# Kernel tuning notes

Hardware: AMD Instinct MI355X
Metric: run time of the kernel (lower is better)

Reference implementation:

```python
import jax, jax.numpy as jnp
import numpy as np

E = 1024      # emb_dim
H = 16        # num_heads
DH = E // H   # per-head atten_dim
B = 2
T = 2048


def _layernorm(x, scale, shift, eps=1e-5):
    mean = x.mean(axis=-1, keepdims=True)
    var = ((x - mean) ** 2).mean(axis=-1, keepdims=True)  # unbiased=False
    return scale * (x - mean) / jnp.sqrt(var + eps) + shift


def _gelu(x):
    # Faithful to source: tanh(sqrt(2/pi)*x + 0.044715*x^3)  (no sqrt on cubic term)
    c = jnp.sqrt(jnp.asarray(2.0 / jnp.pi, x.dtype))
    return 0.5 * x * (1.0 + jnp.tanh(c * x + 0.044715 * x ** 3))


def setup_inputs() -> dict:
    key = jax.random.key(0)
    ks = jax.random.split(key, 12)
    s = 0.02
    return {
        "x":     jax.random.normal(ks[0], (B, T, E), jnp.float32),
        "Wq":    jax.random.normal(ks[1], (H, E, DH), jnp.float32) * s,
        "Wk":    jax.random.normal(ks[2], (H, E, DH), jnp.float32) * s,
        "Wv":    jax.random.normal(ks[3], (H, E, DH), jnp.float32) * s,
        "fc_w":  jax.random.normal(ks[4], (E, E), jnp.float32) * s,
        "fc_b":  jnp.zeros((E,), jnp.float32),
        "ln1_s": jnp.ones((E,), jnp.float32),
        "ln1_b": jnp.zeros((E,), jnp.float32),
        "ln2_s": jnp.ones((E,), jnp.float32),
        "ln2_b": jnp.zeros((E,), jnp.float32),
        "ff_w1": jax.random.normal(ks[5], (E, 4 * E), jnp.float32) * s,
        "ff_b1": jnp.zeros((4 * E,), jnp.float32),
        "ff_w2": jax.random.normal(ks[6], (4 * E, E), jnp.float32) * s,
        "ff_b2": jnp.zeros((E,), jnp.float32),
    }


def _attention(x, Wq, Wk, Wv, fc_w, fc_b):
    b, t, _ = x.shape
    q = jnp.einsum("bte,hed->bhtd", x, Wq)
    k = jnp.einsum("bte,hed->bhtd", x, Wk)
    v = jnp.einsum("bte,hed->bhtd", x, Wv)
    scores = jnp.einsum("bhtd,bhsd->bhts", q, k)
    causal = jnp.triu(jnp.ones((t, t), bool), 1)
    scores = jnp.where(causal, -jnp.inf, scores)
    w = jax.nn.softmax(scores / jnp.sqrt(jnp.asarray(DH, x.dtype)), axis=-1)
    ctx = jnp.einsum("bhts,bhsd->bhtd", w, v)
    # faithful quirk from source: per-head transpose(1,2) then reshape(b, T, d_out)
    ctx = jnp.swapaxes(ctx, 2, 3).reshape(b, H, t, DH)
    concat = ctx.transpose(0, 2, 1, 3).reshape(b, t, E)
    return concat @ fc_w + fc_b


def reference(x, Wq, Wk, Wv, fc_w, fc_b, ln1_s, ln1_b, ln2_s, ln2_b,
              ff_w1, ff_b1, ff_w2, ff_b2):
    h = _attention(_layernorm(x, ln1_s, ln1_b), Wq, Wk, Wv, fc_w, fc_b) + x
    y = _layernorm(h, ln2_s, ln2_b)
    y = _gelu(y @ ff_w1 + ff_b1) @ ff_w2 + ff_b2
    return y + h
```

## Files before the change

### kernel.cpp

```cpp
#include <hip/hip_runtime.h>


#define En 1024
#define Hn 16
#define DHn 64
#define Bn 2
#define Tn 2048
#define Mrows 4096

typedef __attribute__((ext_vector_type(8))) short bf16x8;
typedef __attribute__((ext_vector_type(4))) float f32x4;

__device__ __forceinline__ short f2bf(float f) {
    unsigned u = __float_as_uint(f);
    u += 0x7FFFu + ((u >> 16) & 1u);
    return (short)(u >> 16);
}
__device__ __forceinline__ ushort f2bfu(float f) {
    unsigned u = __float_as_uint(f);
    u += 0x7FFFu + ((u >> 16) & 1u);
    return (ushort)(u >> 16);
}
__device__ __forceinline__ float bf2f(ushort u) {
    return __uint_as_float((unsigned)u << 16);
}

__device__ __forceinline__ float gelu_f(float x) {
    float u = 0.79788456080286535588f * x + 0.044715f * x * x * x;
    float t = __expf(2.0f * u);
    return x * t / (t + 1.0f);
}

__device__ __forceinline__ void load_lds16(const void* g, void* l) {
    __builtin_amdgcn_global_load_lds(
        (const __attribute__((address_space(1))) unsigned int*)(uintptr_t)g,
        (__attribute__((address_space(3))) unsigned int*)(uintptr_t)l,
        16, 0, 0);
}

__global__ __launch_bounds__(256) void ln_kernel(
    const float* __restrict__ in, const float* __restrict__ sc,
    const float* __restrict__ sh, ushort* __restrict__ out)
{
    int row = blockIdx.x;
    int tid = threadIdx.x;
    float4 v = ((const float4*)(in + (size_t)row * En))[tid];
    float s  = v.x + v.y + v.z + v.w;
    float s2 = v.x*v.x + v.y*v.y + v.z*v.z + v.w*v.w;
    #pragma unroll
    for (int off = 32; off > 0; off >>= 1) {
        s  += __shfl_down(s,  off);
        s2 += __shfl_down(s2, off);
    }
    __shared__ float red[2][4];
    int wave = tid >> 6, lane = tid & 63;
    if (lane == 0) { red[0][wave] = s; red[1][wave] = s2; }
    __syncthreads();
    s  = red[0][0] + red[0][1] + red[0][2] + red[0][3];
    s2 = red[1][0] + red[1][1] + red[1][2] + red[1][3];
    float mean = s * (1.0f / En);
    float var  = s2 * (1.0f / En) - mean * mean;
    float r = rsqrtf(var + 1e-5f);
    float4 scv = ((const float4*)sc)[tid];
    float4 shv = ((const float4*)sh)[tid];
    ushort4 o;
    o.x = f2bfu(scv.x * (v.x - mean) * r + shv.x);
    o.y = f2bfu(scv.y * (v.y - mean) * r + shv.y);
    o.z = f2bfu(scv.z * (v.z - mean) * r + shv.z);
    o.w = f2bfu(scv.w * (v.w - mean) * r + shv.w);
    ((ushort4*)(out + (size_t)row * En))[tid] = o;
}

__global__ __launch_bounds__(256) void ln2_fuse(
    const ushort* __restrict__ P0, const ushort* __restrict__ P1,
    const float* __restrict__ bias, const float* __restrict__ x,
    const float* __restrict__ sc, const float* __restrict__ sh,
    ushort* __restrict__ hb, ushort* __restrict__ ynb)
{
    int row = blockIdx.x, tid = threadIdx.x;
    size_t idx = (size_t)row * 256 + tid;
    ushort4 a = ((const ushort4*)P0)[idx];
    ushort4 b = ((const ushort4*)P1)[idx];
    float4 bi = ((const float4*)bias)[tid];
    float4 xr = ((const float4*)x)[idx];
    float4 v;
    v.x = bf2f(a.x) + bf2f(b.x) + bi.x + xr.x;
    v.y = bf2f(a.y) + bf2f(b.y) + bi.y + xr.y;
    v.z = bf2f(a.z) + bf2f(b.z) + bi.z + xr.z;
    v.w = bf2f(a.w) + bf2f(b.w) + bi.w + xr.w;
    ushort4 hv;
    hv.x = f2bfu(v.x); hv.y = f2bfu(v.y); hv.z = f2bfu(v.z); hv.w = f2bfu(v.w);
    ((ushort4*)hb)[idx] = hv;
    float s  = v.x + v.y + v.z + v.w;
    float s2 = v.x*v.x + v.y*v.y + v.z*v.z + v.w*v.w;
    #pragma unroll
    for (int off = 32; off > 0; off >>= 1) {
        s  += __shfl_down(s,  off);
        s2 += __shfl_down(s2, off);
    }
    __shared__ float red[2][4];
    int wave = tid >> 6, lane = tid & 63;
    if (lane == 0) { red[0][wave] = s; red[1][wave] = s2; }
    __syncthreads();
    s  = red[0][0] + red[0][1] + red[0][2] + red[0][3];
    s2 = red[1][0] + red[1][1] + red[1][2] + red[1][3];
    float mean = s * (1.0f / En);
    float var  = s2 * (1.0f / En) - mean * mean;
    float r = rsqrtf(var + 1e-5f);
    float4 scv = ((const float4*)sc)[tid];
    float4 shv = ((const float4*)sh)[tid];
    ushort4 o;
    o.x = f2bfu(scv.x * (v.x - mean) * r + shv.x);
    o.y = f2bfu(scv.y * (v.y - mean) * r + shv.y);
    o.z = f2bfu(scv.z * (v.z - mean) * r + shv.z);
    o.w = f2bfu(scv.w * (v.w - mean) * r + shv.w);
    ((ushort4*)ynb)[idx] = o;
}

__global__ __launch_bounds__(256) void ff2_reduce4(
    const ushort* __restrict__ P, const float* __restrict__ bias,
    const ushort* __restrict__ hb, float* __restrict__ out)
{
    int tid = threadIdx.x;
    size_t i = (size_t)blockIdx.x * 256 + tid;
    const size_t S = (size_t)Mrows * En / 4;
    ushort4 a = ((const ushort4*)P)[i];
    ushort4 b = ((const ushort4*)P)[i + S];
    ushort4 c = ((const ushort4*)P)[i + 2 * S];
    ushort4 d = ((const ushort4*)P)[i + 3 * S];
    float4 bi = ((const float4*)bias)[tid];
    ushort4 hu = ((const ushort4*)hb)[i];
    float4 o;
    o.x = (bf2f(a.x) + bf2f(b.x)) + (bf2f(c.x) + bf2f(d.x)) + bi.x + bf2f(hu.x);
    o.y = (bf2f(a.y) + bf2f(b.y)) + (bf2f(c.y) + bf2f(d.y)) + bi.y + bf2f(hu.y);
    o.z = (bf2f(a.z) + bf2f(b.z)) + (bf2f(c.z) + bf2f(d.z)) + bi.z + bf2f(hu.z);
    o.w = (bf2f(a.w) + bf2f(b.w)) + (bf2f(c.w) + bf2f(d.w)) + bi.w + bf2f(hu.w);
    ((float4*)out)[i] = o;
}

__global__ __launch_bounds__(256) void prep_w(
    const float* __restrict__ Wq, const float* __restrict__ Wk,
    const float* __restrict__ Wv, const float* __restrict__ fc_w,
    const float* __restrict__ ff_w1, const float* __restrict__ ff_w2,
    ushort* __restrict__ wqkv, ushort* __restrict__ wfc,
    ushort* __restrict__ wf1, ushort* __restrict__ wf2)
{
    int bid = blockIdx.x;
    const float* in; ushort* out; int N, ldo, k0, n0;
    if (bid < 768) {
        int z = bid >> 4, kb = bid & 15;
        int sel = z / 16, h = z % 16;
        in  = (sel == 0 ? Wq : sel == 1 ? Wk : Wv) + (size_t)h * En * DHn;
        out = wqkv + (size_t)(sel * 1024 + h * 64) * En;
        N = DHn; ldo = En; k0 = kb * 64; n0 = 0;
    } else if (bid < 1024) {
        int b2 = bid - 768;
        in = fc_w; out = wfc; N = En; ldo = En;
        k0 = (b2 & 15) * 64; n0 = (b2 >> 4) * 64;
    } else if (bid < 2048) {
        int b2 = bid - 1024;
        in = ff_w1; out = wf1; N = 4 * En; ldo = En;
        k0 = (b2 & 15) * 64; n0 = (b2 >> 4) * 64;
    } else {
        int b2 = bid - 2048;
        in = ff_w2; out = wf2; N = En; ldo = 4 * En;
        k0 = (b2 & 63) * 64; n0 = (b2 >> 6) * 64;
    }
    __shared__ float t[64][65];
    int tid = threadIdx.x, r = tid >> 4, c4 = (tid & 15) * 4;
    #pragma unroll
    for (int i = 0; i < 4; ++i) {
        float4 v = *(const float4*)(in + (size_t)(k0 + r + i * 16) * N + n0 + c4);
        t[r + i * 16][c4 + 0] = v.x; t[r + i * 16][c4 + 1] = v.y;
        t[r + i * 16][c4 + 2] = v.z; t[r + i * 16][c4 + 3] = v.w;
    }
    __syncthreads();
    #pragma unroll
    for (int i = 0; i < 4; ++i) {
        int n = r + i * 16;
        ushort4 u;
        u.x = f2bfu(t[c4 + 0][n]); u.y = f2bfu(t[c4 + 1][n]);
        u.z = f2bfu(t[c4 + 2][n]); u.w = f2bfu(t[c4 + 3][n]);
        *(ushort4*)(out + (size_t)(n0 + n) * ldo + k0 + c4) = u;
    }
}

template<int MODE, int TN>
__global__ __launch_bounds__(256) void gemm_bf16(
    const ushort* __restrict__ A, int lda,
    const ushort* __restrict__ Bt, int ldb, int Kloop,
    const float* __restrict__ bias,
    ushort* __restrict__ Cb, int ldc,
    ushort* __restrict__ qo, ushort* __restrict__ ko, ushort* __restrict__ vo)
{
    constexpr int WCN = TN / 2;
    constexpr int NI  = WCN / 16;
    constexpr int BIW = TN * 8 / 256;
    constexpr int STAGE = 128 * 64 + TN * 64;
    constexpr int BOUNCE = (MODE == 2 || MODE == 1) ? 4 * 64 * 68
                         : (MODE == 3 ? 128 * 68 : 0);
    constexpr int SMEMN = STAGE > BOUNCE ? STAGE : BOUNCE;
    __shared__ ushort smem[SMEMN];
    ushort* As = smem;
    ushort* Bs = smem + 128 * 64;
    int tid = threadIdx.x, wv = tid >> 6, lid = tid & 63;
    int m0 = blockIdx.x * 128, n0 = blockIdx.y * TN;
    int koff = blockIdx.z * Kloop;
    int wr = wv >> 1, wc = wv & 1;
    int hm = lid & 15, hk = lid >> 4;

    f32x4 acc[4][NI];
    #pragma unroll
    for (int i = 0; i < 4; ++i)
        #pragma unroll
        for (int j = 0; j < NI; ++j) acc[i][j] = (f32x4){0.f, 0.f, 0.f, 0.f};

    const ushort* Abase = A + (size_t)m0 * lda + koff;
    const ushort* Bbase = Bt + (size_t)n0 * ldb + koff;

    for (int k0 = 0; k0 < Kloop; k0 += 64) {
        __syncthreads();
        #pragma unroll
        for (int i = 0; i < 4; ++i) {
            int c = wv * 256 + i * 64 + lid;
            int r = c >> 3, s = c & 7;
            int j = s ^ (r & 7);
            load_lds16(Abase + (size_t)r * lda + k0 + j * 8,
                       &As[(wv * 256 + i * 64) * 8]);
        }
        #pragma unroll
        for (int i = 0; i < BIW; ++i) {
            int c = wv * (BIW * 64) + i * 64 + lid;
            int r = c >> 3, s = c & 7;
            int j = s ^ (r & 7);
            load_lds16(Bbase + (size_t)r * ldb + k0 + j * 8,
                       &Bs[(wv * (BIW * 64) + i * 64) * 8]);
        }
        __syncthreads();
        #pragma unroll
        for (int kk = 0; kk < 2; ++kk) {
            bf16x8 af[4], bfr[NI];
            #pragma unroll
            for (int mi = 0; mi < 4; ++mi) {
                int r = wr * 64 + mi * 16 + hm;
                int slot = ((kk << 2) | hk) ^ (r & 7);
                af[mi] = *(const bf16x8*)&As[(r * 8 + slot) * 8];
            }
            #pragma unroll
            for (int ni = 0; ni < NI; ++ni) {
                int r = wc * WCN + ni * 16 + hm;
                int slot = ((kk << 2) | hk) ^ (r & 7);
                bfr[ni] = *(const bf16x8*)&Bs[(r * 8 + slot) * 8];
            }
            #pragma unroll
            for (int mi = 0; mi < 4; ++mi)
                #pragma unroll
                for (int ni = 0; ni < NI; ++ni)
                    acc[mi][ni] = __builtin_amdgcn_mfma_f32_16x16x32_bf16(
                        af[mi], bfr[ni], acc[mi][ni], 0, 0, 0);
        }
    }

    int colbase = n0 + wc * WCN + hm;
    int rowbase = m0 + wr * 64 + hk * 4;
    if (MODE == 1) {
        __syncthreads();
        ushort* Ls = smem + wv * (64 * 68);
        #pragma unroll
        for (int ni = 0; ni < NI; ++ni) {
            int col = colbase + ni * 16;
            float bb = bias[col];
            #pragma unroll
            for (int mi = 0; mi < 4; ++mi)
                #pragma unroll
                for (int r = 0; r < 4; ++r)
                    Ls[(mi * 16 + hk * 4 + r) * 68 + ni * 16 + hm] =
                        f2bfu(gelu_f(acc[mi][ni][r] + bb));
        }
        ushort* outp = Cb + (size_t)(m0 + wr * 64) * ldc + n0 + wc * 64;
        int dcol = hm * 4;
        #pragma unroll
        for (int i = 0; i < 16; ++i) {
            int t = hk + i * 4;
            *(ushort4*)(outp + (size_t)t * ldc + dcol) =
                *(const ushort4*)&Ls[t * 68 + dcol];
        }
    } else if (MODE == 2) {
        __syncthreads();
        ushort* Ls = smem + wv * (64 * 68);
        int col0 = n0 + wc * 64;
        int sel = col0 >> 10, h = (col0 & 1023) >> 6;
        if (sel < 2) {
            #pragma unroll
            for (int ni = 0; ni < NI; ++ni)
                #pragma unroll
                for (int mi = 0; mi < 4; ++mi)
                    #pragma unroll
                    for (int r = 0; r < 4; ++r)
                        Ls[(mi * 16 + hk * 4 + r) * 68 + ni * 16 + hm] =
                            f2bfu(acc[mi][ni][r]);
            ushort* outp = (sel == 0 ? qo : ko) + (size_t)h * (Mrows * DHn);
            int dcol = hm * 4;
            #pragma unroll
            for (int i = 0; i < 16; ++i) {
                int t = hk + i * 4;
                *(ushort4*)(outp + (size_t)(m0 + wr * 64 + t) * DHn + dcol) =
                    *(const ushort4*)&Ls[t * 68 + dcol];
            }
        } else {
            #pragma unroll
            for (int ni = 0; ni < NI; ++ni)
                #pragma unroll
                for (int mi = 0; mi < 4; ++mi)
                    #pragma unroll
                    for (int r = 0; r < 4; ++r)
                        Ls[(ni * 16 + hm) * 68 + mi * 16 + hk * 4 + r] =
                            f2bfu(acc[mi][ni][r]);
            int bb2 = m0 >> 11;
            int t0 = (m0 & 2047) + wr * 64;
            ushort* outp = vo + ((size_t)((h * 2 + bb2) * 64)) * Tn + t0;
            int tcol = hm * 4;
            #pragma unroll
            for (int i = 0; i < 16; ++i) {
                int d = hk + i * 4;
                *(ushort4*)(outp + (size_t)d * Tn + tcol) =
                    *(const ushort4*)&Ls[d * 68 + tcol];
            }
        }
    } else {
        __syncthreads();
        ushort* Ls = smem;
        #pragma unroll
        for (int ni = 0; ni < NI; ++ni)
            #pragma unroll
            for (int mi = 0; mi < 4; ++mi)
                #pragma unroll
                for (int r = 0; r < 4; ++r)
                    Ls[(wr * 64 + mi * 16 + hk * 4 + r) * 68
                       + wc * WCN + ni * 16 + hm] = f2bfu(acc[mi][ni][r]);
        __syncthreads();
        ushort* Cp = Cb + (size_t)blockIdx.z * Mrows * ldc;
        #pragma unroll
        for (int it = 0; it < 8; ++it) {
            int i = it * 1024 + tid * 4;
            int row = i >> 6, col = i & 63;
            *(ushort4*)(Cp + (size_t)(m0 + row) * ldc + n0 + col) =
                *(const ushort4*)&Ls[row * 68 + col];
        }
    }
}

#define PHASE_MID() do { \
    __builtin_amdgcn_s_barrier(); \
    asm volatile("s_waitcnt lgkmcnt(0)" ::: "memory"); \
    __builtin_amdgcn_sched_barrier(0); \
} while (0)

#define LOAD_AF(MH, KK) \
    _Pragma("unroll") \
    for (int mi = 0; mi < 4; ++mi) { \
        int r = wr * 128 + (MH) * 64 + mi * 16 + hm; \
        af[mi] = *(const bf16x8*)&As_[(r * 8 + ((((KK) << 2) | hk) ^ (r & 7))) * 8]; \
    }

#define MFMA_PHASE(MH, KK) do { \
    __builtin_amdgcn_s_setprio(1); \
    _Pragma("unroll") \
    for (int mi = 0; mi < 4; ++mi) \
        _Pragma("unroll") \
        for (int ni = 0; ni < 4; ++ni) \
            acc[(MH) * 4 + mi][ni] = __builtin_amdgcn_mfma_f32_16x16x32_bf16( \
                af[mi], bfr[KK][ni], acc[(MH) * 4 + mi][ni], 0, 0, 0); \
    __builtin_amdgcn_s_setprio(0); \
} while (0)

#define STAGE_A(bufp, h, ksrc) do { \
    ushort* _d = smem + (bufp) * 32768; \
    load_lds16(Abase + aoff[h][0] + (ksrc), _d + ldsoff[h][0]); \
    load_lds16(Abase + aoff[h][1] + (ksrc), _d + ldsoff[h][1]); \
} while (0)

#define STAGE_B(bufp, h, ksrc) do { \
    ushort* _d = smem + (bufp) * 32768 + 16384; \
    load_lds16(Bbase + boff[h][0] + (ksrc), _d + ldsoff[h][0]); \
    load_lds16(Bbase + boff[h][1] + (ksrc), _d + ldsoff[h][1]); \
} while (0)

template<int MODE>
__global__ __launch_bounds__(512, 2) void gemm256(
    const ushort* __restrict__ A, int lda,
    const ushort* __restrict__ Bt, int ldb, int Kloop,
    const float* __restrict__ bias,
    ushort* __restrict__ Cb, int ldc,
    ushort* __restrict__ qo, ushort* __restrict__ ko, ushort* __restrict__ vo)
{
    __shared__ ushort smem[65536];
    int tid = threadIdx.x, wv = tid >> 6, lid = tid & 63;
    int wr = wv >> 2, wc = wv & 3;
    int hm = lid & 15, hk = lid >> 4;
    int m0 = blockIdx.x * 256, n0 = blockIdx.y * 256;
    int koff = blockIdx.z * Kloop;
    int NT = Kloop >> 6;

    const ushort* Abase = A + (size_t)m0 * lda + koff;
    const ushort* Bbase = Bt + (size_t)n0 * ldb + koff;

    int aoff[2][2], boff[2][2], ldsoff[2][2];
    #pragma unroll
    for (int h = 0; h < 2; ++h)
        #pragma unroll
        for (int i = 0; i < 2; ++i) {
            int c = h * 1024 + wv * 128 + i * 64 + lid;
            int r = c >> 3, s = c & 7, j = s ^ (r & 7);
            aoff[h][i] = r * lda + j * 8;
            boff[h][i] = r * ldb + j * 8;
            ldsoff[h][i] = (h * 1024 + wv * 128 + i * 64) * 8;
        }

    f32x4 acc[8][4];
    #pragma unroll
    for (int i = 0; i < 8; ++i)
        #pragma unroll
        for (int j = 0; j < 4; ++j) acc[i][j] = (f32x4){0.f, 0.f, 0.f, 0.f};

    STAGE_A(0, 0, 0); STAGE_A(0, 1, 0);
    STAGE_B(0, 0, 0); STAGE_B(0, 1, 0);
    {
        int k1 = (NT > 1 ? 1 : 0) << 6;
        STAGE_B(1, 0, k1); STAGE_B(1, 1, k1);
    }
    asm volatile("s_waitcnt vmcnt(4)" ::: "memory");
    __builtin_amdgcn_s_barrier();

    for (int t = 0; t < NT; ++t) {
        int cur = t & 1, nxt = cur ^ 1;
        int kA = (t + 1 < NT ? t + 1 : NT - 1) << 6;
        int kB = (t + 2 < NT ? t + 2 : NT - 1) << 6;
        const ushort* As_ = smem + cur * 32768;
        const ushort* Bs_ = As_ + 16384;
        bf16x8 af[4], bfr[2][4];

        LOAD_AF(0, 0);
        #pragma unroll
        for (int kk = 0; kk < 2; ++kk)
            #pragma unroll
            for (int ni = 0; ni < 4; ++ni) {
                int r = wc * 64 + ni * 16 + hm;
                bfr[kk][ni] = *(const bf16x8*)
                    &Bs_[(r * 8 + (((kk << 2) | hk) ^ (r & 7))) * 8];
            }
        STAGE_A(nxt, 0, kA);
        PHASE_MID();
        MFMA_PHASE(0, 0);
        __builtin_amdgcn_s_barrier();

        LOAD_AF(1, 0);
        STAGE_A(nxt, 1, kA);
        PHASE_MID();
        MFMA_PHASE(1, 0);
        __builtin_amdgcn_s_barrier();

        LOAD_AF(0, 1);
        STAGE_B(cur, 0, kB);
        PHASE_MID();
        MFMA_PHASE(0, 1);
        __builtin_amdgcn_s_barrier();

        LOAD_AF(1, 1);
        STAGE_B(cur, 1, kB);
        PHASE_MID();
        MFMA_PHASE(1, 1);
        asm volatile("s_waitcnt vmcnt(4)" ::: "memory");
        __builtin_amdgcn_s_barrier();
    }
    asm volatile("s_waitcnt vmcnt(0)" ::: "memory");
    __builtin_amdgcn_s_barrier();

    ushort* Ls = smem + wv * (64 * 68);
    int dcol = hm * 4;
    if (MODE == 1) {
        float bb[4];
        #pragma unroll
        for (int ni = 0; ni < 4; ++ni) bb[ni] = bias[n0 + wc * 64 + ni * 16 + hm];
        #pragma unroll
        for (int mh = 0; mh < 2; ++mh) {
            #pragma unroll
            for (int ni = 0; ni < 4; ++ni)
                #pragma unroll
                for (int mi = 0; mi < 4; ++mi)
                    #pragma unroll
                    for (int r = 0; r < 4; ++r)
                        Ls[(mi * 16 + hk * 4 + r) * 68 + ni * 16 + hm] =
                            f2bfu(gelu_f(acc[mh * 4 + mi][ni][r] + bb[ni]));
            ushort* outp = Cb + (size_t)(m0 + wr * 128 + mh * 64) * ldc
                              + n0 + wc * 64;
            #pragma unroll
            for (int i = 0; i < 16; ++i) {
                int tt = hk + i * 4;
                *(ushort4*)(outp + (size_t)tt * ldc + dcol) =
                    *(const ushort4*)&Ls[tt * 68 + dcol];
            }
        }
    } else if (MODE == 2) {
        int col0 = n0 + wc * 64;
        int sel = col0 >> 10, hh = (col0 & 1023) >> 6;
        #pragma unroll
        for (int mh = 0; mh < 2; ++mh) {
            int rowb = m0 + wr * 128 + mh * 64;
            if (sel < 2) {
                #pragma unroll
                for (int ni = 0; ni < 4; ++ni)
                    #pragma unroll
                    for (int mi = 0; mi < 4; ++mi)
                        #pragma unroll
                        for (int r = 0; r < 4; ++r)
                            Ls[(mi * 16 + hk * 4 + r) * 68 + ni * 16 + hm] =
                                f2bfu(acc[mh * 4 + mi][ni][r]);
                ushort* outp = (sel == 0 ? qo : ko) + (size_t)hh * (Mrows * DHn);
                #pragma unroll
                for (int i = 0; i < 16; ++i) {
                    int tt = hk + i * 4;
                    *(ushort4*)(outp + (size_t)(rowb + tt) * DHn + dcol) =
                        *(const ushort4*)&Ls[tt * 68 + dcol];
                }
            } else {
                #pragma unroll
                for (int ni = 0; ni < 4; ++ni)
                    #pragma unroll
                    for (int mi = 0; mi < 4; ++mi)
                        #pragma unroll
                        for (int r = 0; r < 4; ++r)
                            Ls[(ni * 16 + hm) * 68 + mi * 16 + hk * 4 + r] =
                                f2bfu(acc[mh * 4 + mi][ni][r]);
                int bb2 = m0 >> 11;
                int t0 = (m0 & 2047) + wr * 128 + mh * 64;
                ushort* outp = vo + ((size_t)((hh * 2 + bb2) * 64)) * Tn + t0;
                #pragma unroll
                for (int i = 0; i < 16; ++i) {
                    int d = hk + i * 4;
                    *(ushort4*)(outp + (size_t)d * Tn + dcol) =
                        *(const ushort4*)&Ls[d * 68 + dcol];
                }
            }
        }
    } else {
        ushort* Cp = Cb + (size_t)blockIdx.z * ((size_t)Mrows * ldc);
        #pragma unroll
        for (int mh = 0; mh < 2; ++mh) {
            #pragma unroll
            for (int ni = 0; ni < 4; ++ni)
                #pragma unroll
                for (int mi = 0; mi < 4; ++mi)
                    #pragma unroll
                    for (int r = 0; r < 4; ++r)
                        Ls[(mi * 16 + hk * 4 + r) * 68 + ni * 16 + hm] =
                            f2bfu(acc[mh * 4 + mi][ni][r]);
            ushort* outp = Cp + (size_t)(m0 + wr * 128 + mh * 64) * ldc
                              + n0 + wc * 64;
            #pragma unroll
            for (int i = 0; i < 16; ++i) {
                int tt = hk + i * 4;
                *(ushort4*)(outp + (size_t)tt * ldc + dcol) =
                    *(const ushort4*)&Ls[tt * 68 + dcol];
            }
        }
    }
}

__global__ __launch_bounds__(256) void attn_mfma(
    const ushort* __restrict__ q, const ushort* __restrict__ ksrc,
    const ushort* __restrict__ vtsrc, ushort* __restrict__ cat)
{
    int g = blockIdx.x;
    int h = g >> 1, b = g & 1;
    const ushort* qg  = q     + (size_t)g * Tn * DHn;
    const ushort* kg  = ksrc  + (size_t)g * Tn * DHn;
    const ushort* vtg = vtsrc + (size_t)g * DHn * Tn;
    int tid = threadIdx.x, wave = tid >> 6, lane = tid & 63;
    int m = lane & 15, gq = lane >> 4;

    __shared__ short Ks[4096];
    __shared__ short Vt[4096];
    __shared__ short Ps[4][1024];

    int R  = tid >> 2;
    int c2 = tid & 3;

    #pragma unroll 1
    for (int phase = 0; phase < 2; ++phase) {
        int qt = phase ? (31 - (int)blockIdx.y) : (int)blockIdx.y;
        int q0 = qt * 64;

        bf16x8 qf[2];
        {
            const ushort* qp = qg + (size_t)(q0 + wave * 16 + m) * DHn + gq * 8;
            qf[0] = *(const bf16x8*)(qp);
            qf[1] = *(const bf16x8*)(qp + 32);
        }
        f32x4 o[4];
        #pragma unroll
        for (int i = 0; i < 4; ++i) o[i] = (f32x4){0.f, 0.f, 0.f, 0.f};
        float lsum[4] = {0.f, 0.f, 0.f, 0.f};

        for (int kt = 0; kt <= qt; ++kt) {
            int k0 = kt * 64;
            __syncthreads();
            {
                const ushort* ksp = kg  + (size_t)(k0 + R) * DHn + c2 * 16;
                const ushort* vsp = vtg + (size_t)R * Tn + k0 + c2 * 16;
                bf16x8 f0 = *(const bf16x8*)(ksp);
                bf16x8 f1 = *(const bf16x8*)(ksp + 8);
                bf16x8 v0 = *(const bf16x8*)(vsp);
                bf16x8 v1 = *(const bf16x8*)(vsp + 8);
                *(bf16x8*)&Ks[R * 64 + (((c2 * 2    ) ^ (R & 7)) << 3)] = f0;
                *(bf16x8*)&Ks[R * 64 + (((c2 * 2 + 1) ^ (R & 7)) << 3)] = f1;
                *(bf16x8*)&Vt[R * 64 + (((c2 * 2    ) ^ (R & 7)) << 3)] = v0;
                *(bf16x8*)&Vt[R * 64 + (((c2 * 2 + 1) ^ (R & 7)) << 3)] = v1;
            }
            __syncthreads();

            bool diag = (kt == qt);
            float ps[4][4];
            #pragma unroll
            for (int ct = 0; ct < 4; ++ct) {
                if (diag && ct > wave) {
                    ps[ct][0] = ps[ct][1] = ps[ct][2] = ps[ct][3] = 0.f;
                    continue;
                }
                f32x4 acc = (f32x4){0.f, 0.f, 0.f, 0.f};
                int row = ct * 16 + m;
                #pragma unroll
                for (int db = 0; db < 2; ++db) {
                    bf16x8 kf = *(const bf16x8*)&Ks[row * 64 + (((db * 4 + gq) ^ (row & 7)) << 3)];
                    acc = __builtin_amdgcn_mfma_f32_16x16x32_bf16(qf[db], kf, acc, 0, 0, 0);
                }
                #pragma unroll
                for (int r = 0; r < 4; ++r) {
                    float p;
                    if (diag && (ct * 16 + m) > (wave * 16 + gq * 4 + r)) {
                        p = 0.f;
                    } else {
                        p = __expf(acc[r] * 0.125f);
                    }
                    ps[ct][r] = p;
                    lsum[r] += p;
                }
            }

            #pragma unroll
            for (int ct = 0; ct < 4; ++ct)
                #pragma unroll
                for (int r = 0; r < 4; ++r) {
                    int row = gq * 4 + r;
                    Ps[wave][row * 64 + ((((ct * 2 + (m >> 3)) ^ (row & 7)) << 3) | (m & 7))] =
                        f2bf(ps[ct][r]);
                }
            bf16x8 pf[2];
            #pragma unroll
            for (int db2 = 0; db2 < 2; ++db2)
                pf[db2] = *(const bf16x8*)&Ps[wave][m * 64 + (((db2 * 4 + gq) ^ (m & 7)) << 3)];

            #pragma unroll
            for (int ct2 = 0; ct2 < 4; ++ct2) {
                int row = ct2 * 16 + m;
                #pragma unroll
                for (int db2 = 0; db2 < 2; ++db2) {
                    bf16x8 vf = *(const bf16x8*)&Vt[row * 64 + (((db2 * 4 + gq) ^ (row & 7)) << 3)];
                    o[ct2] = __builtin_amdgcn_mfma_f32_16x16x32_bf16(pf[db2], vf, o[ct2], 0, 0, 0);
                }
            }
        }

        float inv[4];
        #pragma unroll
        for (int r = 0; r < 4; ++r) {
            float l = lsum[r];
            l += __shfl_xor(l, 1);
            l += __shfl_xor(l, 2);
            l += __shfl_xor(l, 4);
            l += __shfl_xor(l, 8);
            inv[r] = 1.0f / l;
        }
        size_t base = (size_t)b * Tn * En + (size_t)h * 64 + (size_t)qt * En
                    + wave * 16 + gq * 4;
        #pragma unroll
        for (int ct2 = 0; ct2 < 4; ++ct2) {
            int d = ct2 * 16 + m;
            #pragma unroll
            for (int r = 0; r < 4; ++r)
                cat[base + (size_t)d * 32 * En + r] = f2bfu(o[ct2][r] * inv[r]);
        }
    }
}

extern "C" void kernel_launch(void* const* d_in, const int* in_sizes, int n_in,
                              void* d_out, int out_size, void* d_ws, size_t ws_size,
                              hipStream_t stream) {
    const float* x     = (const float*)d_in[0];
    const float* Wq    = (const float*)d_in[1];
    const float* Wk    = (const float*)d_in[2];
    const float* Wv    = (const float*)d_in[3];
    const float* fc_w  = (const float*)d_in[4];
    const float* fc_b  = (const float*)d_in[5];
    const float* ln1_s = (const float*)d_in[6];
    const float* ln1_b = (const float*)d_in[7];
    const float* ln2_s = (const float*)d_in[8];
    const float* ln2_b = (const float*)d_in[9];
    const float* ff_w1 = (const float*)d_in[10];
    const float* ff_b1 = (const float*)d_in[11];
    const float* ff_w2 = (const float*)d_in[12];
    const float* ff_b2 = (const float*)d_in[13];
    float* out = (float*)d_out;
    (void)in_sizes; (void)n_in; (void)out_size; (void)ws_size;

    const size_t MB = 1048576;
    char* w8 = (char*)d_ws;
    ushort* S0   = (ushort*)(w8 + 0 * MB);
    ushort* kb   = (ushort*)(w8 + 8 * MB);
    ushort* vtb  = (ushort*)(w8 + 16 * MB);
    ushort* qb   = (ushort*)(w8 + 24 * MB);
    ushort* hb   = (ushort*)(w8 + 32 * MB);
    ushort* Pfc  = (ushort*)(w8 + 48 * MB);
    ushort* y1   = (ushort*)(w8 + 48 * MB);
    ushort* Pff2 = (ushort*)(w8 + 0 * MB);
    ushort* wqkv = (ushort*)(w8 + 80 * MB);
    ushort* wfc  = (ushort*)(w8 + 86 * MB);
    ushort* wf1  = (ushort*)(w8 + 88 * MB);
    ushort* wf2  = (ushort*)(w8 + 96 * MB);

    prep_w<<<dim3(3072), 256, 0, stream>>>(
        Wq, Wk, Wv, fc_w, ff_w1, ff_w2, wqkv, wfc, wf1, wf2);

    ln_kernel<<<dim3(Mrows), 256, 0, stream>>>(x, ln1_s, ln1_b, S0);
    gemm256<2><<<dim3(16, 12), 512, 0, stream>>>(
        S0, En, wqkv, En, En, nullptr, nullptr, 0, qb, kb, vtb);
    attn_mfma<<<dim3(Hn * Bn, 16), 256, 0, stream>>>(qb, kb, vtb, S0);
    gemm_bf16<3, 64><<<dim3(32, 16, 2), 256, 0, stream>>>(
        S0, En, wfc, En, En / 2, nullptr, Pfc, En, nullptr, nullptr, nullptr);
    ln2_fuse<<<dim3(Mrows), 256, 0, stream>>>(
        Pfc, Pfc + (size_t)Mrows * En, fc_b, x, ln2_s, ln2_b, hb, qb);
    gemm256<1><<<dim3(16, 16), 512, 0, stream>>>(
        qb, En, wf1, En, En, ff_b1, y1, 4 * En, nullptr, nullptr, nullptr);
    gemm256<3><<<dim3(16, 4, 4), 512, 0, stream>>>(
        y1, 4 * En, wf2, 4 * En, En, nullptr, Pff2, En, nullptr, nullptr, nullptr);
    ff2_reduce4<<<dim3(Mrows), 256, 0, stream>>>(Pff2, ff_b2, hb, out);
}
```

Measured before the change: 330.5 us.

## Double-buffer K/V tiles and widen attention blocks to 128 query rows

The attention kernel now uses 512 threads (8 waves) per block covering 128 query rows. K/V tiles are double-buffered in LDS, with the next tile prefetched into registers while the current one is consumed, which cuts the per-tile barriers from two to one. MFMA sections are wrapped in s_setprio to favour matrix issue. The cost is half as many blocks in the grid (256 instead of 512), more LDS per block, and waves on the diagonal sitting idle for partially masked tiles.

```diff
diff --git a/kernel.cpp b/kernel.cpp
--- a/kernel.cpp
+++ b/kernel.cpp
@@ -567,7 +567,7 @@
     }
 }
 
-__global__ __launch_bounds__(256) void attn_mfma(
+__global__ __launch_bounds__(512) void attn_mfma(
     const ushort* __restrict__ q, const ushort* __restrict__ ksrc,
     const ushort* __restrict__ vtsrc, ushort* __restrict__ cat)
 {
@@ -576,24 +576,29 @@
     const ushort* qg  = q     + (size_t)g * Tn * DHn;
     const ushort* kg  = ksrc  + (size_t)g * Tn * DHn;
     const ushort* vtg = vtsrc + (size_t)g * DHn * Tn;
-    int tid = threadIdx.x, wave = tid >> 6, lane = tid & 63;
+    int tid = threadIdx.x, w = tid >> 6, lane = tid & 63;
     int m = lane & 15, gq = lane >> 4;
 
-    __shared__ short Ks[4096];
-    __shared__ short Vt[4096];
-    __shared__ short Ps[4][1024];
-
-    int R  = tid >> 2;
-    int c2 = tid & 3;
+    __shared__ short Ks[2][4096];
+    __shared__ short Vt[2][4096];
+    __shared__ short Ps[8][1024];
+
+    int R = tid >> 3;
+    int c = tid & 7;
+    int slot = R * 64 + ((c ^ (R & 7)) << 3);
+    const ushort* kbase = kg  + (size_t)R * DHn + c * 8;
+    const ushort* vbase = vtg + (size_t)R * Tn  + c * 8;
 
     #pragma unroll 1
     for (int phase = 0; phase < 2; ++phase) {
-        int qt = phase ? (31 - (int)blockIdx.y) : (int)blockIdx.y;
-        int q0 = qt * 64;
+        int qj = phase ? (15 - (int)blockIdx.y) : (int)blockIdx.y;
+        int q0 = qj * 128;
+        int NT = 2 * qj + 2;
+        int qb = q0 + w * 16;
 
         bf16x8 qf[2];
         {
-            const ushort* qp = qg + (size_t)(q0 + wave * 16 + m) * DHn + gq * 8;
+            const ushort* qp = qg + (size_t)(qb + m) * DHn + gq * 8;
             qf[0] = *(const bf16x8*)(qp);
             qf[1] = *(const bf16x8*)(qp + 32);
         }
@@ -602,73 +607,84 @@
         for (int i = 0; i < 4; ++i) o[i] = (f32x4){0.f, 0.f, 0.f, 0.f};
         float lsum[4] = {0.f, 0.f, 0.f, 0.f};
 
-        for (int kt = 0; kt <= qt; ++kt) {
-            int k0 = kt * 64;
+        bf16x8 kreg = *(const bf16x8*)(kbase);
+        bf16x8 vreg = *(const bf16x8*)(vbase);
+        *(bf16x8*)&Ks[0][slot] = kreg;
+        *(bf16x8*)&Vt[0][slot] = vreg;
+        __syncthreads();
+
+        #pragma unroll 1
+        for (int kt = 0; kt < NT; ++kt) {
+            int cur = kt & 1;
+            if (kt + 1 < NT) {
+                kreg = *(const bf16x8*)(kbase + (size_t)(kt + 1) * 4096);
+                vreg = *(const bf16x8*)(vbase + (kt + 1) * 64);
+            }
+            if (qb >= kt * 64) {
+                float ps[4][4];
+                #pragma unroll
+                for (int ct = 0; ct < 4; ++ct) {
+                    int dk = kt * 64 + ct * 16 - qb;
+                    if (dk > 0) {
+                        ps[ct][0] = ps[ct][1] = ps[ct][2] = ps[ct][3] = 0.f;
+                        continue;
+                    }
+                    f32x4 acc = (f32x4){0.f, 0.f, 0.f, 0.f};
+                    int row = ct * 16 + m;
+                    __builtin_amdgcn_s_setprio(1);
+                    #pragma unroll
+                    for (int db = 0; db < 2; ++db) {
+                        bf16x8 kf = *(const bf16x8*)
+                            &Ks[cur][row * 64 + (((db * 4 + gq) ^ (row & 7)) << 3)];
+                        acc = __builtin_amdgcn_mfma_f32_16x16x32_bf16(
+                            qf[db], kf, acc, 0, 0, 0);
+                    }
+                    __builtin_amdgcn_s_setprio(0);
+                    #pragma unroll
+                    for (int r = 0; r < 4; ++r) {
+                        float p;
+                        if (dk == 0 && m > gq * 4 + r) p = 0.f;
+                        else p = __expf(acc[r] * 0.125f);
+                        ps[ct][r] = p;
+                        lsum[r] += p;
+                    }
+                }
+
+                #pragma unroll
+                for (int ct = 0; ct < 4; ++ct)
+                    #pragma unroll
+                    for (int r = 0; r < 4; ++r) {
+                        int prow = gq * 4 + r;
+                        Ps[w][prow * 64 +
+                              ((((ct * 2 + (m >> 3)) ^ (prow & 7)) << 3) | (m & 7))] =
+                            f2bf(ps[ct][r]);
+                    }
+                bf16x8 pf[2];
+                #pragma unroll
+                for (int db2 = 0; db2 < 2; ++db2)
+                    pf[db2] = *(const bf16x8*)
+                        &Ps[w][m * 64 + (((db2 * 4 + gq) ^ (m & 7)) << 3)];
+
+                __builtin_amdgcn_s_setprio(1);
+                #pragma unroll
+                for (int ct2 = 0; ct2 < 4; ++ct2) {
+                    int row = ct2 * 16 + m;
+                    #pragma unroll
+                    for (int db2 = 0; db2 < 2; ++db2) {
+                        bf16x8 vf = *(const bf16x8*)
+                            &Vt[cur][row * 64 + (((db2 * 4 + gq) ^ (row & 7)) << 3)];
+                        o[ct2] = __builtin_amdgcn_mfma_f32_16x16x32_bf16(
+                            pf[db2], vf, o[ct2], 0, 0, 0);
+                    }
+                }
+                __builtin_amdgcn_s_setprio(0);
+            }
+            if (kt + 1 < NT) {
+                int nb = (kt + 1) & 1;
+                *(bf16x8*)&Ks[nb][slot] = kreg;
+                *(bf16x8*)&Vt[nb][slot] = vreg;
+            }
             __syncthreads();
-            {
-                const ushort* ksp = kg  + (size_t)(k0 + R) * DHn + c2 * 16;
-                const ushort* vsp = vtg + (size_t)R * Tn + k0 + c2 * 16;
-                bf16x8 f0 = *(const bf16x8*)(ksp);
-                bf16x8 f1 = *(const bf16x8*)(ksp + 8);
-                bf16x8 v0 = *(const bf16x8*)(vsp);
-                bf16x8 v1 = *(const bf16x8*)(vsp + 8);
-                *(bf16x8*)&Ks[R * 64 + (((c2 * 2    ) ^ (R & 7)) << 3)] = f0;
-                *(bf16x8*)&Ks[R * 64 + (((c2 * 2 + 1) ^ (R & 7)) << 3)] = f1;
-                *(bf16x8*)&Vt[R * 64 + (((c2 * 2    ) ^ (R & 7)) << 3)] = v0;
-                *(bf16x8*)&Vt[R * 64 + (((c2 * 2 + 1) ^ (R & 7)) << 3)] = v1;
-            }
-            __syncthreads();
-
-            bool diag = (kt == qt);
-            float ps[4][4];
-            #pragma unroll
-            for (int ct = 0; ct < 4; ++ct) {
-                if (diag && ct > wave) {
-                    ps[ct][0] = ps[ct][1] = ps[ct][2] = ps[ct][3] = 0.f;
-                    continue;
-                }
-                f32x4 acc = (f32x4){0.f, 0.f, 0.f, 0.f};
-                int row = ct * 16 + m;
-                #pragma unroll
-                for (int db = 0; db < 2; ++db) {
-                    bf16x8 kf = *(const bf16x8*)&Ks[row * 64 + (((db * 4 + gq) ^ (row & 7)) << 3)];
-                    acc = __builtin_amdgcn_mfma_f32_16x16x32_bf16(qf[db], kf, acc, 0, 0, 0);
-                }
-                #pragma unroll
-                for (int r = 0; r < 4; ++r) {
-                    float p;
-                    if (diag && (ct * 16 + m) > (wave * 16 + gq * 4 + r)) {
-                        p = 0.f;
-                    } else {
-                        p = __expf(acc[r] * 0.125f);
-                    }
-                    ps[ct][r] = p;
-                    lsum[r] += p;
-                }
-            }
-
-            #pragma unroll
-            for (int ct = 0; ct < 4; ++ct)
-                #pragma unroll
-                for (int r = 0; r < 4; ++r) {
-                    int row = gq * 4 + r;
-                    Ps[wave][row * 64 + ((((ct * 2 + (m >> 3)) ^ (row & 7)) << 3) | (m & 7))] =
-                        f2bf(ps[ct][r]);
-                }
-            bf16x8 pf[2];
-            #pragma unroll
-            for (int db2 = 0; db2 < 2; ++db2)
-                pf[db2] = *(const bf16x8*)&Ps[wave][m * 64 + (((db2 * 4 + gq) ^ (m & 7)) << 3)];
-
-            #pragma unroll
-            for (int ct2 = 0; ct2 < 4; ++ct2) {
-                int row = ct2 * 16 + m;
-                #pragma unroll
-                for (int db2 = 0; db2 < 2; ++db2) {
-                    bf16x8 vf = *(const bf16x8*)&Vt[row * 64 + (((db2 * 4 + gq) ^ (row & 7)) << 3)];
-                    o[ct2] = __builtin_amdgcn_mfma_f32_16x16x32_bf16(pf[db2], vf, o[ct2], 0, 0, 0);
-                }
-            }
         }
 
         float inv[4];
@@ -681,8 +697,10 @@
             l += __shfl_xor(l, 8);
             inv[r] = 1.0f / l;
         }
-        size_t base = (size_t)b * Tn * En + (size_t)h * 64 + (size_t)qt * En
-                    + wave * 16 + gq * 4;
+        int qt_old = (q0 >> 6) + (w >> 2);
+        int wv_old = w & 3;
+        size_t base = (size_t)b * Tn * En + (size_t)h * 64 + (size_t)qt_old * En
+                    + wv_old * 16 + gq * 4;
         #pragma unroll
         for (int ct2 = 0; ct2 < 4; ++ct2) {
             int d = ct2 * 16 + m;
@@ -734,7 +752,7 @@
     ln_kernel<<<dim3(Mrows), 256, 0, stream>>>(x, ln1_s, ln1_b, S0);
     gemm256<2><<<dim3(16, 12), 512, 0, stream>>>(
         S0, En, wqkv, En, En, nullptr, nullptr, 0, qb, kb, vtb);
-    attn_mfma<<<dim3(Hn * Bn, 16), 256, 0, stream>>>(qb, kb, vtb, S0);
+    attn_mfma<<<dim3(Hn * Bn, 8), 512, 0, stream>>>(qb, kb, vtb, S0);
     gemm_bf16<3, 64><<<dim3(32, 16, 2), 256, 0, stream>>>(
         S0, En, wfc, En, En / 2, nullptr, Pfc, En, nullptr, nullptr, nullptr);
     ln2_fuse<<<dim3(Mrows), 256, 0, stream>>>(
```

Measured after the change: 324.2 us. Within noise of the previous version (-1.9%).
